# Kernel optimization log

Hardware: AMD Instinct MI355X
Metric: run time of the kernel (lower is better)

## Reference

```python
import jax, jax.numpy as jnp
import numpy as np

D_MODEL = 1024
NUM_HEADS = 16
DEPTH = D_MODEL // NUM_HEADS


def setup_inputs() -> dict:
    key = jax.random.key(0)
    ks = jax.random.split(key, 9)
    s = 1.0 / np.sqrt(D_MODEL)
    return {
        "inputs": jax.random.normal(ks[0], (2, 2048, D_MODEL), dtype=jnp.float32),
        "wq": jax.random.normal(ks[1], (D_MODEL, D_MODEL), dtype=jnp.float32) * s,
        "bq": jnp.zeros((D_MODEL,), dtype=jnp.float32),
        "wk": jax.random.normal(ks[2], (D_MODEL, D_MODEL), dtype=jnp.float32) * s,
        "bk": jnp.zeros((D_MODEL,), dtype=jnp.float32),
        "wv": jax.random.normal(ks[3], (D_MODEL, D_MODEL), dtype=jnp.float32) * s,
        "bv": jnp.zeros((D_MODEL,), dtype=jnp.float32),
        "wo": jax.random.normal(ks[4], (D_MODEL, D_MODEL), dtype=jnp.float32) * s,
        "bo": jnp.zeros((D_MODEL,), dtype=jnp.float32),
    }


def _split_heads(x, B, S):
    # [B, S, d_model] -> [B, H, S, depth]
    return x.reshape(B, S, NUM_HEADS, DEPTH).transpose(0, 2, 1, 3)


def reference(inputs, wq, bq, wk, bk, wv, bv, wo, bo):
    B, S, _ = inputs.shape
    q = _split_heads(inputs @ wq + bq, B, S)
    k = _split_heads(inputs @ wk + bk, B, S)
    v = _split_heads(inputs @ wv + bv, B, S)
    scale = 1.0 / jnp.sqrt(jnp.asarray(DEPTH, dtype=inputs.dtype))
    logits = jnp.einsum("bhqd,bhkd->bhqk", q, k) * scale
    attn = jax.nn.softmax(logits, axis=-1)  # [B, H, S, S]
    ctx = jnp.einsum("bhqk,bhkd->bhqd", attn, v)
    ctx = ctx.transpose(0, 2, 1, 3).reshape(B, S, D_MODEL)
    out = ctx @ wo + bo
    return out, attn
```

## Files before the change

### kernel.cpp

```cpp
#include <hip/hip_runtime.h>

typedef _Float16 f16;
typedef _Float16 f16x8 __attribute__((ext_vector_type(8)));
typedef _Float16 f16x4 __attribute__((ext_vector_type(4)));
typedef float f32x4 __attribute__((ext_vector_type(4)));

#define MFMA16(a, b, c) __builtin_amdgcn_mfma_f32_16x16x32_f16((a), (b), (c), 0, 0, 0)

constexpr int DM = 1024;
constexpr int NH = 16;
constexpr int DEPTH = 64;
constexpr int SEQ = 2048;
constexpr int BATCH = 2;
constexpr int MTOT = BATCH * SEQ;

__global__ void k_cvt(const float* __restrict__ x, f16* __restrict__ y, int n) {
  int i = (blockIdx.x * blockDim.x + threadIdx.x) * 4;
  if (i >= n) return;
  const float4 v = *(const float4*)(x + i);
  f16x4 h;
  h[0] = (f16)v.x; h[1] = (f16)v.y; h[2] = (f16)v.z; h[3] = (f16)v.w;
  *(f16x4*)(y + i) = h;
}

template <int MODE>
__global__ __launch_bounds__(256) void k_gemm(const f16* __restrict__ A,
                                              const float* __restrict__ Bw,
                                              const float* __restrict__ bias,
                                              void* __restrict__ outp) {
  constexpr int K = DM, N = DM;
  __shared__ f16 Al[128 * 32];
  __shared__ f16 Bl[128 * 32];
  const int tid = threadIdx.x;
  const int lane = tid & 63;
  const int wave = tid >> 6;
  const int m0 = blockIdx.y * 128;
  const int n0 = blockIdx.x * 128;
  const int wr = (wave >> 1) * 64;
  const int wc = (wave & 1) * 64;
  const int lr = lane & 15;
  const int lk = (lane >> 4) * 8;

  f32x4 acc[4][4];
  for (int i = 0; i < 4; i++)
    for (int j = 0; j < 4; j++) acc[i][j] = (f32x4)0.0f;

  const int ar = tid >> 1, ak = (tid & 1) * 16;
  const int bn = (tid & 31) * 4, bk = (tid >> 5) * 4;

  for (int k0 = 0; k0 < K; k0 += 32) {
    __syncthreads();
    const f16* ag = A + (size_t)(m0 + ar) * K + k0 + ak;
    f16x8 a0 = *(const f16x8*)(ag);
    f16x8 a1 = *(const f16x8*)(ag + 8);
    *(f16x8*)(Al + ar * 32 + ak) = a0;
    *(f16x8*)(Al + ar * 32 + ak + 8) = a1;
    float4 w[4];
    for (int i = 0; i < 4; i++)
      w[i] = *(const float4*)(Bw + (size_t)(k0 + bk + i) * N + n0 + bn);
    for (int j = 0; j < 4; j++) {
      f16x4 h;
      h[0] = (f16)(((const float*)&w[0])[j]);
      h[1] = (f16)(((const float*)&w[1])[j]);
      h[2] = (f16)(((const float*)&w[2])[j]);
      h[3] = (f16)(((const float*)&w[3])[j]);
      *(f16x4*)(Bl + (size_t)(bn + j) * 32 + bk) = h;
    }
    __syncthreads();
    f16x8 af[4], bf[4];
    for (int i = 0; i < 4; i++)
      af[i] = *(const f16x8*)(Al + (wr + i * 16 + lr) * 32 + lk);
    for (int j = 0; j < 4; j++)
      bf[j] = *(const f16x8*)(Bl + (wc + j * 16 + lr) * 32 + lk);
    for (int i = 0; i < 4; i++)
      for (int j = 0; j < 4; j++) acc[i][j] = MFMA16(af[i], bf[j], acc[i][j]);
  }

  for (int j = 0; j < 4; j++) {
    const int n = n0 + wc + j * 16 + lr;
    const float bv = bias[n];
    for (int i = 0; i < 4; i++) {
      for (int r = 0; r < 4; r++) {
        const int m = m0 + wr + i * 16 + (lane >> 4) * 4 + r;
        const float val = acc[i][j][r] + bv;
        if (MODE == 1) {
          ((float*)outp)[(size_t)m * N + n] = val;
        } else {
          const int b = m >> 11, s = m & 2047;
          const int h = n >> 6, d = n & 63;
          size_t idx;
          if (MODE == 0)
            idx = ((size_t)(b * NH + h) * SEQ + s) * DEPTH + d;
          else
            idx = ((size_t)(b * NH + h) * DEPTH + d) * SEQ + s;
          ((f16*)outp)[idx] = (f16)val;
        }
      }
    }
  }
}

__global__ __launch_bounds__(256) void k_attn(const f16* __restrict__ qws,
                                              const f16* __restrict__ kws,
                                              const f16* __restrict__ vtws,
                                              float* __restrict__ attn,
                                              f16* __restrict__ ctx) {
  __shared__ f16 Qs[64 * 64];
  __shared__ f16 Ks[64 * 64];
  __shared__ f16 Vs[64 * 64];
  __shared__ f16 Ps[4][16 * 64];

  const int tid = threadIdx.x, lane = tid & 63, wave = tid >> 6;
  const int bh = blockIdx.y;
  const int q0 = blockIdx.x * 64;
  const int lr = lane & 15, lk = (lane >> 4) * 8;

  const f16* qb = qws + (size_t)bh * SEQ * DEPTH;
  const f16* kb = kws + (size_t)bh * SEQ * DEPTH;
  const f16* vb = vtws + (size_t)bh * DEPTH * SEQ;

  const int sr = tid >> 2, sc = (tid & 3) * 16;
  *(f16x8*)(Qs + sr * 64 + sc)     = *(const f16x8*)(qb + (size_t)(q0 + sr) * 64 + sc);
  *(f16x8*)(Qs + sr * 64 + sc + 8) = *(const f16x8*)(qb + (size_t)(q0 + sr) * 64 + sc + 8);
  __syncthreads();
  f16x8 qf0 = *(const f16x8*)(Qs + (wave * 16 + lr) * 64 + lk);
  f16x8 qf1 = *(const f16x8*)(Qs + (wave * 16 + lr) * 64 + 32 + lk);

  float rs[4] = {0.f, 0.f, 0.f, 0.f};
  for (int kt = 0; kt < SEQ; kt += 64) {
    __syncthreads();
    *(f16x8*)(Ks + sr * 64 + sc)     = *(const f16x8*)(kb + (size_t)(kt + sr) * 64 + sc);
    *(f16x8*)(Ks + sr * 64 + sc + 8) = *(const f16x8*)(kb + (size_t)(kt + sr) * 64 + sc + 8);
    __syncthreads();
    for (int nb = 0; nb < 4; nb++) {
      f32x4 a = (f32x4)0.0f;
      f16x8 b0 = *(const f16x8*)(Ks + (nb * 16 + lr) * 64 + lk);
      f16x8 b1 = *(const f16x8*)(Ks + (nb * 16 + lr) * 64 + 32 + lk);
      a = MFMA16(qf0, b0, a);
      a = MFMA16(qf1, b1, a);
      for (int r = 0; r < 4; r++) rs[r] += __expf(a[r] * 0.125f);
    }
  }
  for (int r = 0; r < 4; r++) {
    float v = rs[r];
    v += __shfl_xor(v, 1);
    v += __shfl_xor(v, 2);
    v += __shfl_xor(v, 4);
    v += __shfl_xor(v, 8);
    rs[r] = 1.0f / v;
  }

  f32x4 cacc[4];
  for (int d = 0; d < 4; d++) cacc[d] = (f32x4)0.0f;
  float* ab = attn + (size_t)bh * SEQ * SEQ;

  for (int kt = 0; kt < SEQ; kt += 64) {
    __syncthreads();
    *(f16x8*)(Ks + sr * 64 + sc)     = *(const f16x8*)(kb + (size_t)(kt + sr) * 64 + sc);
    *(f16x8*)(Ks + sr * 64 + sc + 8) = *(const f16x8*)(kb + (size_t)(kt + sr) * 64 + sc + 8);
    *(f16x8*)(Vs + sr * 64 + sc)     = *(const f16x8*)(vb + (size_t)sr * SEQ + kt + sc);
    *(f16x8*)(Vs + sr * 64 + sc + 8) = *(const f16x8*)(vb + (size_t)sr * SEQ + kt + sc + 8);
    __syncthreads();
    for (int nb = 0; nb < 4; nb++) {
      f32x4 a = (f32x4)0.0f;
      f16x8 b0 = *(const f16x8*)(Ks + (nb * 16 + lr) * 64 + lk);
      f16x8 b1 = *(const f16x8*)(Ks + (nb * 16 + lr) * 64 + 32 + lk);
      a = MFMA16(qf0, b0, a);
      a = MFMA16(qf1, b1, a);
      for (int r = 0; r < 4; r++) {
        const float p = __expf(a[r] * 0.125f) * rs[r];
        const int qrow = wave * 16 + (lane >> 4) * 4 + r;
        ab[(size_t)(q0 + qrow) * SEQ + kt + nb * 16 + lr] = p;
        Ps[wave][((lane >> 4) * 4 + r) * 64 + nb * 16 + lr] = (f16)p;
      }
    }
    __syncthreads();
    for (int ks = 0; ks < 2; ks++) {
      f16x8 pf = *(const f16x8*)(Ps[wave] + lr * 64 + ks * 32 + lk);
      for (int d = 0; d < 4; d++) {
        f16x8 vf = *(const f16x8*)(Vs + (d * 16 + lr) * 64 + ks * 32 + lk);
        cacc[d] = MFMA16(pf, vf, cacc[d]);
      }
    }
  }

  const int b = bh >> 4, h = bh & 15;
  for (int d = 0; d < 4; d++) {
    for (int r = 0; r < 4; r++) {
      const int qrow = q0 + wave * 16 + (lane >> 4) * 4 + r;
      ctx[(size_t)(b * SEQ + qrow) * DM + h * DEPTH + d * 16 + lr] = (f16)cacc[d][r];
    }
  }
}

extern "C" void kernel_launch(void* const* d_in, const int* in_sizes, int n_in,
                              void* d_out, int out_size, void* d_ws, size_t ws_size,
                              hipStream_t stream) {
  const float* X  = (const float*)d_in[0];
  const float* wq = (const float*)d_in[1];
  const float* bq = (const float*)d_in[2];
  const float* wk = (const float*)d_in[3];
  const float* bk = (const float*)d_in[4];
  const float* wv = (const float*)d_in[5];
  const float* bv = (const float*)d_in[6];
  const float* wo = (const float*)d_in[7];
  const float* bo = (const float*)d_in[8];

  char* ws = (char*)d_ws;
  f16* Xh  = (f16*)(ws);
  f16* Qw  = (f16*)(ws + ((size_t)8 << 20));
  f16* Kw  = (f16*)(ws + ((size_t)16 << 20));
  f16* Vw  = (f16*)(ws + ((size_t)24 << 20));
  f16* Ctx = (f16*)(ws + ((size_t)32 << 20));

  float* out  = (float*)d_out;
  float* attn = out + (size_t)MTOT * DM;

  k_cvt<<<dim3(MTOT * DM / 1024), dim3(256), 0, stream>>>(X, Xh, MTOT * DM);
  dim3 gg(DM / 128, MTOT / 128);
  k_gemm<0><<<gg, 256, 0, stream>>>(Xh, wq, bq, (void*)Qw);
  k_gemm<0><<<gg, 256, 0, stream>>>(Xh, wk, bk, (void*)Kw);
  k_gemm<2><<<gg, 256, 0, stream>>>(Xh, wv, bv, (void*)Vw);
  k_attn<<<dim3(SEQ / 64, BATCH * NH), 256, 0, stream>>>(Qw, Kw, Vw, attn, Ctx);
  k_gemm<1><<<gg, 256, 0, stream>>>(Ctx, wo, bo, (void*)out);
}
```

Baseline: 883.7 us.

## Prefetch tiles into registers, swizzle LDS, batch QKV GEMMs, vectorize attn stores

Adds register prefetch of the next K-tile in both the GEMM and attention loops so global loads overlap with the MFMA work. Applies XOR swizzles to the LDS layouts to avoid bank conflicts. Merges the three QKV projections into one launch with a z-dimension. Swaps MFMA operand order in attention so each lane owns one query row, which allows a single scalar row sum and vectorized nontemporal float4 stores of the attention matrix. The per-block branch on z adds a runtime mode selection, and the register prefetch raises register pressure.

```diff
diff --git a/kernel.cpp b/kernel.cpp
--- a/kernel.cpp
+++ b/kernel.cpp
@@ -13,6 +13,13 @@
 constexpr int SEQ = 2048;
 constexpr int BATCH = 2;
 constexpr int MTOT = BATCH * SEQ;
+
+__device__ __forceinline__ int swzA(int row, int off) {
+  return row * 64 + (off ^ ((row & 7) << 3));
+}
+__device__ __forceinline__ int swzG(int row, int off) {
+  return row * 32 + (off ^ (((row >> 1) & 3) << 3));
+}
 
 __global__ void k_cvt(const float* __restrict__ x, f16* __restrict__ y, int n) {
   int i = (blockIdx.x * blockDim.x + threadIdx.x) * 4;
@@ -23,14 +30,26 @@
   *(f16x4*)(y + i) = h;
 }
 
-template <int MODE>
-__global__ __launch_bounds__(256) void k_gemm(const f16* __restrict__ A,
-                                              const float* __restrict__ Bw,
-                                              const float* __restrict__ bias,
-                                              void* __restrict__ outp) {
+template <int FINAL>
+__global__ __launch_bounds__(256, 3) void k_gemm(const f16* __restrict__ A,
+                                                 const float* __restrict__ B0,
+                                                 const float* __restrict__ B1,
+                                                 const float* __restrict__ B2,
+                                                 const float* __restrict__ bias0,
+                                                 const float* __restrict__ bias1,
+                                                 const float* __restrict__ bias2,
+                                                 void* __restrict__ o0,
+                                                 void* __restrict__ o1,
+                                                 void* __restrict__ o2) {
   constexpr int K = DM, N = DM;
   __shared__ f16 Al[128 * 32];
   __shared__ f16 Bl[128 * 32];
+  const int z = blockIdx.z;
+  const float* Bw   = FINAL ? B0 : (z == 0 ? B0 : (z == 1 ? B1 : B2));
+  const float* bias = FINAL ? bias0 : (z == 0 ? bias0 : (z == 1 ? bias1 : bias2));
+  void* outp        = FINAL ? o0 : (z == 0 ? o0 : (z == 1 ? o1 : o2));
+  const int mode = FINAL ? 1 : (z == 2 ? 2 : 0);
+
   const int tid = threadIdx.x;
   const int lane = tid & 63;
   const int wave = tid >> 6;
@@ -48,30 +67,47 @@
   const int ar = tid >> 1, ak = (tid & 1) * 16;
   const int bn = (tid & 31) * 4, bk = (tid >> 5) * 4;
 
+  f16x8 a0r, a1r;
+  float4 w0, w1, w2, w3;
+  {
+    const f16* ag = A + (size_t)(m0 + ar) * K + ak;
+    a0r = *(const f16x8*)(ag);
+    a1r = *(const f16x8*)(ag + 8);
+    const float* bg = Bw + (size_t)bk * N + n0 + bn;
+    w0 = *(const float4*)(bg);
+    w1 = *(const float4*)(bg + N);
+    w2 = *(const float4*)(bg + 2 * N);
+    w3 = *(const float4*)(bg + 3 * N);
+  }
+
   for (int k0 = 0; k0 < K; k0 += 32) {
     __syncthreads();
-    const f16* ag = A + (size_t)(m0 + ar) * K + k0 + ak;
-    f16x8 a0 = *(const f16x8*)(ag);
-    f16x8 a1 = *(const f16x8*)(ag + 8);
-    *(f16x8*)(Al + ar * 32 + ak) = a0;
-    *(f16x8*)(Al + ar * 32 + ak + 8) = a1;
-    float4 w[4];
-    for (int i = 0; i < 4; i++)
-      w[i] = *(const float4*)(Bw + (size_t)(k0 + bk + i) * N + n0 + bn);
+    *(f16x8*)(Al + swzG(ar, ak))     = a0r;
+    *(f16x8*)(Al + swzG(ar, ak + 8)) = a1r;
     for (int j = 0; j < 4; j++) {
       f16x4 h;
-      h[0] = (f16)(((const float*)&w[0])[j]);
-      h[1] = (f16)(((const float*)&w[1])[j]);
-      h[2] = (f16)(((const float*)&w[2])[j]);
-      h[3] = (f16)(((const float*)&w[3])[j]);
-      *(f16x4*)(Bl + (size_t)(bn + j) * 32 + bk) = h;
-    }
-    __syncthreads();
+      h[0] = (f16)(((const float*)&w0)[j]);
+      h[1] = (f16)(((const float*)&w1)[j]);
+      h[2] = (f16)(((const float*)&w2)[j]);
+      h[3] = (f16)(((const float*)&w3)[j]);
+      *(f16x4*)(Bl + swzG(bn + j, bk)) = h;
+    }
+    __syncthreads();
+    if (k0 + 32 < K) {
+      const f16* ag = A + (size_t)(m0 + ar) * K + (k0 + 32) + ak;
+      a0r = *(const f16x8*)(ag);
+      a1r = *(const f16x8*)(ag + 8);
+      const float* bg = Bw + (size_t)(k0 + 32 + bk) * N + n0 + bn;
+      w0 = *(const float4*)(bg);
+      w1 = *(const float4*)(bg + N);
+      w2 = *(const float4*)(bg + 2 * N);
+      w3 = *(const float4*)(bg + 3 * N);
+    }
     f16x8 af[4], bf[4];
     for (int i = 0; i < 4; i++)
-      af[i] = *(const f16x8*)(Al + (wr + i * 16 + lr) * 32 + lk);
+      af[i] = *(const f16x8*)(Al + swzG(wr + i * 16 + lr, lk));
     for (int j = 0; j < 4; j++)
-      bf[j] = *(const f16x8*)(Bl + (wc + j * 16 + lr) * 32 + lk);
+      bf[j] = *(const f16x8*)(Bl + swzG(wc + j * 16 + lr, lk));
     for (int i = 0; i < 4; i++)
       for (int j = 0; j < 4; j++) acc[i][j] = MFMA16(af[i], bf[j], acc[i][j]);
   }
@@ -83,13 +119,13 @@
       for (int r = 0; r < 4; r++) {
         const int m = m0 + wr + i * 16 + (lane >> 4) * 4 + r;
         const float val = acc[i][j][r] + bv;
-        if (MODE == 1) {
+        if (mode == 1) {
           ((float*)outp)[(size_t)m * N + n] = val;
         } else {
           const int b = m >> 11, s = m & 2047;
           const int h = n >> 6, d = n & 63;
           size_t idx;
-          if (MODE == 0)
+          if (mode == 0)
             idx = ((size_t)(b * NH + h) * SEQ + s) * DEPTH + d;
           else
             idx = ((size_t)(b * NH + h) * DEPTH + d) * SEQ + s;
@@ -113,72 +149,105 @@
   const int tid = threadIdx.x, lane = tid & 63, wave = tid >> 6;
   const int bh = blockIdx.y;
   const int q0 = blockIdx.x * 64;
-  const int lr = lane & 15, lk = (lane >> 4) * 8;
+  const int lr = lane & 15, g = lane >> 4, lk = g * 8;
 
   const f16* qb = qws + (size_t)bh * SEQ * DEPTH;
   const f16* kb = kws + (size_t)bh * SEQ * DEPTH;
   const f16* vb = vtws + (size_t)bh * DEPTH * SEQ;
 
   const int sr = tid >> 2, sc = (tid & 3) * 16;
-  *(f16x8*)(Qs + sr * 64 + sc)     = *(const f16x8*)(qb + (size_t)(q0 + sr) * 64 + sc);
-  *(f16x8*)(Qs + sr * 64 + sc + 8) = *(const f16x8*)(qb + (size_t)(q0 + sr) * 64 + sc + 8);
+  {
+    const f16* qg = qb + (size_t)(q0 + sr) * 64 + sc;
+    *(f16x8*)(Qs + swzA(sr, sc))     = *(const f16x8*)(qg);
+    *(f16x8*)(Qs + swzA(sr, sc + 8)) = *(const f16x8*)(qg + 8);
+  }
   __syncthreads();
-  f16x8 qf0 = *(const f16x8*)(Qs + (wave * 16 + lr) * 64 + lk);
-  f16x8 qf1 = *(const f16x8*)(Qs + (wave * 16 + lr) * 64 + 32 + lk);
-
-  float rs[4] = {0.f, 0.f, 0.f, 0.f};
+  const f16x8 qf0 = *(const f16x8*)(Qs + swzA(wave * 16 + lr, lk));
+  const f16x8 qf1 = *(const f16x8*)(Qs + swzA(wave * 16 + lr, 32 + lk));
+
+  f16x8 kr0, kr1;
+  {
+    const f16* kg = kb + (size_t)sr * 64 + sc;
+    kr0 = *(const f16x8*)(kg);
+    kr1 = *(const f16x8*)(kg + 8);
+  }
+  float rsum = 0.f;
   for (int kt = 0; kt < SEQ; kt += 64) {
     __syncthreads();
-    *(f16x8*)(Ks + sr * 64 + sc)     = *(const f16x8*)(kb + (size_t)(kt + sr) * 64 + sc);
-    *(f16x8*)(Ks + sr * 64 + sc + 8) = *(const f16x8*)(kb + (size_t)(kt + sr) * 64 + sc + 8);
-    __syncthreads();
+    *(f16x8*)(Ks + swzA(sr, sc))     = kr0;
+    *(f16x8*)(Ks + swzA(sr, sc + 8)) = kr1;
+    __syncthreads();
+    if (kt + 64 < SEQ) {
+      const f16* kg = kb + (size_t)(kt + 64 + sr) * 64 + sc;
+      kr0 = *(const f16x8*)(kg);
+      kr1 = *(const f16x8*)(kg + 8);
+    }
     for (int nb = 0; nb < 4; nb++) {
       f32x4 a = (f32x4)0.0f;
-      f16x8 b0 = *(const f16x8*)(Ks + (nb * 16 + lr) * 64 + lk);
-      f16x8 b1 = *(const f16x8*)(Ks + (nb * 16 + lr) * 64 + 32 + lk);
-      a = MFMA16(qf0, b0, a);
-      a = MFMA16(qf1, b1, a);
-      for (int r = 0; r < 4; r++) rs[r] += __expf(a[r] * 0.125f);
-    }
-  }
-  for (int r = 0; r < 4; r++) {
-    float v = rs[r];
-    v += __shfl_xor(v, 1);
-    v += __shfl_xor(v, 2);
-    v += __shfl_xor(v, 4);
-    v += __shfl_xor(v, 8);
-    rs[r] = 1.0f / v;
-  }
+      f16x8 kf0 = *(const f16x8*)(Ks + swzA(nb * 16 + lr, lk));
+      f16x8 kf1 = *(const f16x8*)(Ks + swzA(nb * 16 + lr, 32 + lk));
+      a = MFMA16(kf0, qf0, a);
+      a = MFMA16(kf1, qf1, a);
+      rsum += (__expf(a[0] * 0.125f) + __expf(a[1] * 0.125f)) +
+              (__expf(a[2] * 0.125f) + __expf(a[3] * 0.125f));
+    }
+  }
+  rsum += __shfl_xor(rsum, 16);
+  rsum += __shfl_xor(rsum, 32);
+  const float rsinv = 1.0f / rsum;
 
   f32x4 cacc[4];
   for (int d = 0; d < 4; d++) cacc[d] = (f32x4)0.0f;
-  float* ab = attn + (size_t)bh * SEQ * SEQ;
+  float* ab = attn + (size_t)bh * SEQ * SEQ + (size_t)(q0 + wave * 16 + lr) * SEQ + g * 4;
+
+  f16x8 vr0, vr1;
+  {
+    const f16* kg = kb + (size_t)sr * 64 + sc;
+    kr0 = *(const f16x8*)(kg);
+    kr1 = *(const f16x8*)(kg + 8);
+    const f16* vg = vb + (size_t)sr * SEQ + sc;
+    vr0 = *(const f16x8*)(vg);
+    vr1 = *(const f16x8*)(vg + 8);
+  }
+  f16* Psw = Ps[wave];
 
   for (int kt = 0; kt < SEQ; kt += 64) {
     __syncthreads();
-    *(f16x8*)(Ks + sr * 64 + sc)     = *(const f16x8*)(kb + (size_t)(kt + sr) * 64 + sc);
-    *(f16x8*)(Ks + sr * 64 + sc + 8) = *(const f16x8*)(kb + (size_t)(kt + sr) * 64 + sc + 8);
-    *(f16x8*)(Vs + sr * 64 + sc)     = *(const f16x8*)(vb + (size_t)sr * SEQ + kt + sc);
-    *(f16x8*)(Vs + sr * 64 + sc + 8) = *(const f16x8*)(vb + (size_t)sr * SEQ + kt + sc + 8);
-    __syncthreads();
+    *(f16x8*)(Ks + swzA(sr, sc))     = kr0;
+    *(f16x8*)(Ks + swzA(sr, sc + 8)) = kr1;
+    *(f16x8*)(Vs + swzA(sr, sc))     = vr0;
+    *(f16x8*)(Vs + swzA(sr, sc + 8)) = vr1;
+    __syncthreads();
+    if (kt + 64 < SEQ) {
+      const f16* kg = kb + (size_t)(kt + 64 + sr) * 64 + sc;
+      kr0 = *(const f16x8*)(kg);
+      kr1 = *(const f16x8*)(kg + 8);
+      const f16* vg = vb + (size_t)sr * SEQ + kt + 64 + sc;
+      vr0 = *(const f16x8*)(vg);
+      vr1 = *(const f16x8*)(vg + 8);
+    }
     for (int nb = 0; nb < 4; nb++) {
       f32x4 a = (f32x4)0.0f;
-      f16x8 b0 = *(const f16x8*)(Ks + (nb * 16 + lr) * 64 + lk);
-      f16x8 b1 = *(const f16x8*)(Ks + (nb * 16 + lr) * 64 + 32 + lk);
-      a = MFMA16(qf0, b0, a);
-      a = MFMA16(qf1, b1, a);
-      for (int r = 0; r < 4; r++) {
-        const float p = __expf(a[r] * 0.125f) * rs[r];
-        const int qrow = wave * 16 + (lane >> 4) * 4 + r;
-        ab[(size_t)(q0 + qrow) * SEQ + kt + nb * 16 + lr] = p;
-        Ps[wave][((lane >> 4) * 4 + r) * 64 + nb * 16 + lr] = (f16)p;
-      }
+      f16x8 kf0 = *(const f16x8*)(Ks + swzA(nb * 16 + lr, lk));
+      f16x8 kf1 = *(const f16x8*)(Ks + swzA(nb * 16 + lr, 32 + lk));
+      a = MFMA16(kf0, qf0, a);
+      a = MFMA16(kf1, qf1, a);
+      const float p0 = __expf(a[0] * 0.125f) * rsinv;
+      const float p1 = __expf(a[1] * 0.125f) * rsinv;
+      const float p2 = __expf(a[2] * 0.125f) * rsinv;
+      const float p3 = __expf(a[3] * 0.125f) * rsinv;
+      f32x4 pq;
+      pq[0] = p0; pq[1] = p1; pq[2] = p2; pq[3] = p3;
+      __builtin_nontemporal_store(pq, (f32x4*)(ab + kt + nb * 16));
+      f16x4 ph;
+      ph[0] = (f16)p0; ph[1] = (f16)p1; ph[2] = (f16)p2; ph[3] = (f16)p3;
+      *(f16x4*)(Psw + swzA(lr, nb * 16 + g * 4)) = ph;
     }
     __syncthreads();
     for (int ks = 0; ks < 2; ks++) {
-      f16x8 pf = *(const f16x8*)(Ps[wave] + lr * 64 + ks * 32 + lk);
+      f16x8 pf = *(const f16x8*)(Psw + swzA(lr, ks * 32 + lk));
       for (int d = 0; d < 4; d++) {
-        f16x8 vf = *(const f16x8*)(Vs + (d * 16 + lr) * 64 + ks * 32 + lk);
+        f16x8 vf = *(const f16x8*)(Vs + swzA(d * 16 + lr, ks * 32 + lk));
         cacc[d] = MFMA16(pf, vf, cacc[d]);
       }
     }
@@ -187,7 +256,7 @@
   const int b = bh >> 4, h = bh & 15;
   for (int d = 0; d < 4; d++) {
     for (int r = 0; r < 4; r++) {
-      const int qrow = q0 + wave * 16 + (lane >> 4) * 4 + r;
+      const int qrow = q0 + wave * 16 + g * 4 + r;
       ctx[(size_t)(b * SEQ + qrow) * DM + h * DEPTH + d * 16 + lr] = (f16)cacc[d][r];
     }
   }
@@ -217,10 +286,9 @@
   float* attn = out + (size_t)MTOT * DM;
 
   k_cvt<<<dim3(MTOT * DM / 1024), dim3(256), 0, stream>>>(X, Xh, MTOT * DM);
-  dim3 gg(DM / 128, MTOT / 128);
-  k_gemm<0><<<gg, 256, 0, stream>>>(Xh, wq, bq, (void*)Qw);
-  k_gemm<0><<<gg, 256, 0, stream>>>(Xh, wk, bk, (void*)Kw);
-  k_gemm<2><<<gg, 256, 0, stream>>>(Xh, wv, bv, (void*)Vw);
+  k_gemm<0><<<dim3(DM / 128, MTOT / 128, 3), 256, 0, stream>>>(
+      Xh, wq, wk, wv, bq, bk, bv, (void*)Qw, (void*)Kw, (void*)Vw);
   k_attn<<<dim3(SEQ / 64, BATCH * NH), 256, 0, stream>>>(Qw, Kw, Vw, attn, Ctx);
-  k_gemm<1><<<gg, 256, 0, stream>>>(Ctx, wo, bo, (void*)out);
-}
+  k_gemm<1><<<dim3(DM / 128, MTOT / 128, 1), 256, 0, stream>>>(
+      Ctx, wo, wo, wo, bo, bo, bo, (void*)out, (void*)out, (void*)out);
+}
```

After: 766.4 us. 1.15x faster.
